# Optimization experiments

Hardware: AMD Instinct MI355X
Metric: run time of the kernel (lower is better)

The kernel has to match this reference:

```python
import jax, jax.numpy as jnp
import numpy as np

B, C, H, W = 64, 3, 512, 512


def setup_inputs() -> dict:
    key = jax.random.key(0)
    k_img, k_w, k_h, k_x, k_y = jax.random.split(key, 5)
    images = jax.random.normal(k_img, (B, C, H, W), dtype=jnp.float32)
    widths = jax.random.randint(k_w, (B,), 0, 256, dtype=jnp.int32)
    heights = jax.random.randint(k_h, (B,), 0, 256, dtype=jnp.int32)
    xs = jax.random.randint(k_x, (B,), 0, W, dtype=jnp.int32)
    ys = jax.random.randint(k_y, (B,), 0, H, dtype=jnp.int32)
    return {"images": images, "widths": widths, "heights": heights, "xs": xs, "ys": ys}


def reference(images, widths, heights, xs, ys):
    # Build [B, H, W] rectangle mask on-device (no per-image host sync):
    # mask[i, y:y+h, x:x+w] = 1, equivalent to torch slice-assign loop.
    rows = jnp.arange(H, dtype=jnp.int32)[None, :, None]  # [1, H, 1]
    cols = jnp.arange(W, dtype=jnp.int32)[None, None, :]  # [1, 1, W]
    y0 = ys[:, None, None]
    x0 = xs[:, None, None]
    in_rect = (
        (rows >= y0) & (rows < y0 + heights[:, None, None])
        & (cols >= x0) & (cols < x0 + widths[:, None, None])
    )  # [B, H, W]
    keep = jnp.where(in_rect, 0.0, 1.0).astype(images.dtype)
    return images * keep[:, None, :, :]
```

## Files before the change

kernel.cpp:

```cpp
#include <hip/hip_runtime.h>


typedef float f32x4 __attribute__((ext_vector_type(4)));

constexpr int Hc = 512, Wc = 512;
constexpr int VPR    = Wc / 4;
constexpr int TOTAL  = 64 * 3 * Hc * VPR;
constexpr int BLOCKS = 2048, THREADS = 256;
constexpr int STRIDE = BLOCKS * THREADS;
constexpr int ITERS  = TOTAL / STRIDE;

static_assert(TOTAL % STRIDE == 0, "clean tiling");

__global__ __launch_bounds__(THREADS) void erase_kernel(
    const f32x4* __restrict__ in, f32x4* __restrict__ out,
    const int* __restrict__ xs, const int* __restrict__ ys,
    const int* __restrict__ wd, const int* __restrict__ ht)
{
    const int base = blockIdx.x * THREADS + threadIdx.x;

    #pragma unroll
    for (int it = 0; it < ITERS; ++it) {
        const int idx = base + it * STRIDE;
        const int img = idx >> 16;
        const int b   = img / 3;
        const int h   = (idx >> 7) & (Hc - 1);
        const int w   = (idx & (VPR - 1)) << 2;

        const int x0 = xs[b];
        const int y0 = ys[b];
        const int x1 = x0 + wd[b];
        const int y1 = y0 + ht[b];

        const bool in_row = (h >= y0) && (h < y1);

        f32x4 v;
        if (in_row && (w >= x0) && (w + 4 <= x1)) {
            v = (f32x4){0.f, 0.f, 0.f, 0.f};
        } else {
            v = in[idx];
            if (in_row) {
                if (w + 0 >= x0 && w + 0 < x1) v.x = 0.f;
                if (w + 1 >= x0 && w + 1 < x1) v.y = 0.f;
                if (w + 2 >= x0 && w + 2 < x1) v.z = 0.f;
                if (w + 3 >= x0 && w + 3 < x1) v.w = 0.f;
            }
        }
        __builtin_nontemporal_store(v, &out[idx]);
    }
}

extern "C" void kernel_launch(void* const* d_in, const int* in_sizes, int n_in,
                              void* d_out, int out_size, void* d_ws, size_t ws_size,
                              hipStream_t stream) {
    const f32x4* in  = (const f32x4*)d_in[0];
    const int*   wd  = (const int*)d_in[1];
    const int*   ht  = (const int*)d_in[2];
    const int*   xs  = (const int*)d_in[3];
    const int*   ys  = (const int*)d_in[4];
    f32x4*       out = (f32x4*)d_out;

    erase_kernel<<<BLOCKS, THREADS, 0, stream>>>(in, out, xs, ys, wd, ht);
}
```

Baseline: 64.70 us.

## Map blocks to contiguous image chunks and batch loads before stores

Reassigns work so each block covers a contiguous 2048-vector chunk of a single image, instead of a grid-stride layout. Per-image rectangle parameters and the column masks are then computed once per thread, not once per iteration. All eight loads are issued before a scheduling barrier and then all eight stores, which raises memory-level parallelism. The grid grows from 2048 to 6144 blocks, with fewer vectors handled per thread.

```diff
diff --git a/kernel.cpp b/kernel.cpp
--- a/kernel.cpp
+++ b/kernel.cpp
@@ -6,47 +6,65 @@
 constexpr int Hc = 512, Wc = 512;
 constexpr int VPR    = Wc / 4;
 constexpr int TOTAL  = 64 * 3 * Hc * VPR;
-constexpr int BLOCKS = 2048, THREADS = 256;
-constexpr int STRIDE = BLOCKS * THREADS;
-constexpr int ITERS  = TOTAL / STRIDE;
-
-static_assert(TOTAL % STRIDE == 0, "clean tiling");
+constexpr int THREADS = 256;
+constexpr int BATCH   = 8;
+constexpr int PER_BLK = THREADS * BATCH;
+constexpr int BLOCKS  = TOTAL / PER_BLK;
+constexpr int BLK_PER_IMG = (Hc * VPR) / PER_BLK;
 
 __global__ __launch_bounds__(THREADS) void erase_kernel(
     const f32x4* __restrict__ in, f32x4* __restrict__ out,
     const int* __restrict__ xs, const int* __restrict__ ys,
     const int* __restrict__ wd, const int* __restrict__ ht)
 {
-    const int base = blockIdx.x * THREADS + threadIdx.x;
+    const int img = blockIdx.x >> 5;
+    const int b   = img / 3;
+
+    const int x0 = xs[b];
+    const int y0 = ys[b];
+    const int x1 = x0 + wd[b];
+    const int y1 = y0 + ht[b];
+
+    const int t = threadIdx.x;
+    const int w = (t & (VPR - 1)) << 2;
+    const bool mx0 = (w + 0 >= x0) && (w + 0 < x1);
+    const bool mx1 = (w + 1 >= x0) && (w + 1 < x1);
+    const bool mx2 = (w + 2 >= x0) && (w + 2 < x1);
+    const bool mx3 = (w + 3 >= x0) && (w + 3 < x1);
+    const bool full_x = mx0 && mx1 && mx2 && mx3;
+
+    const int base = blockIdx.x * PER_BLK + t;
+    const int h0   = (base >> 7) & (Hc - 1);
+
+    bool in_row[BATCH];
+    #pragma unroll
+    for (int k = 0; k < BATCH; ++k) {
+        const int h = h0 + 2 * k;
+        in_row[k] = (h >= y0) && (h < y1);
+    }
+
+    f32x4 v[BATCH];
+    #pragma unroll
+    for (int k = 0; k < BATCH; ++k) {
+        v[k] = (f32x4){0.f, 0.f, 0.f, 0.f};
+        if (!(in_row[k] && full_x))
+            v[k] = in[base + k * THREADS];
+    }
+    __builtin_amdgcn_sched_barrier(0);
 
     #pragma unroll
-    for (int it = 0; it < ITERS; ++it) {
-        const int idx = base + it * STRIDE;
-        const int img = idx >> 16;
-        const int b   = img / 3;
-        const int h   = (idx >> 7) & (Hc - 1);
-        const int w   = (idx & (VPR - 1)) << 2;
+    for (int k = 0; k < BATCH; ++k) {
+        if (in_row[k]) {
+            if (mx0) v[k].x = 0.f;
+            if (mx1) v[k].y = 0.f;
+            if (mx2) v[k].z = 0.f;
+            if (mx3) v[k].w = 0.f;
+        }
+    }
 
-        const int x0 = xs[b];
-        const int y0 = ys[b];
-        const int x1 = x0 + wd[b];
-        const int y1 = y0 + ht[b];
-
-        const bool in_row = (h >= y0) && (h < y1);
-
-        f32x4 v;
-        if (in_row && (w >= x0) && (w + 4 <= x1)) {
-            v = (f32x4){0.f, 0.f, 0.f, 0.f};
-        } else {
-            v = in[idx];
-            if (in_row) {
-                if (w + 0 >= x0 && w + 0 < x1) v.x = 0.f;
-                if (w + 1 >= x0 && w + 1 < x1) v.y = 0.f;
-                if (w + 2 >= x0 && w + 2 < x1) v.z = 0.f;
-                if (w + 3 >= x0 && w + 3 < x1) v.w = 0.f;
-            }
-        }
-        __builtin_nontemporal_store(v, &out[idx]);
+    #pragma unroll
+    for (int k = 0; k < BATCH; ++k) {
+        __builtin_nontemporal_store(v[k], &out[base + k * THREADS]);
     }
 }
 
```

New measurement: 67.42 us. +4.2%, slower.
